# Kernel optimization log

Measured on AMD Instinct MI355X. Metric: run time of the kernel, lower is better.

The kernel has to match this reference:

```python
import jax, jax.numpy as jnp
import numpy as np

N = 50000
E = 800000
IN_C, HID, OUT_C, HEADS = 128, 32, 64, 4
NEG_SLOPE = 0.2


def setup_inputs() -> dict:
    key = jax.random.key(0)
    ks = jax.random.split(key, 10)
    x = jax.random.normal(ks[0], (N, IN_C), dtype=jnp.float32)
    edge_index = jax.random.randint(ks[1], (2, E), 0, N, dtype=jnp.int64)
    s = 0.05
    W1 = jax.random.normal(ks[2], (IN_C, HID), dtype=jnp.float32) * s
    b1 = jnp.zeros((HID,), dtype=jnp.float32)
    Wg = jax.random.normal(ks[3], (HID, HEADS * HID), dtype=jnp.float32) * s
    ag_src = jax.random.normal(ks[4], (HEADS, HID), dtype=jnp.float32) * s
    ag_dst = jax.random.normal(ks[5], (HEADS, HID), dtype=jnp.float32) * s
    bg = jnp.zeros((HID,), dtype=jnp.float32)
    W2 = jax.random.normal(ks[6], (HID, OUT_C), dtype=jnp.float32) * s
    b2 = jnp.zeros((OUT_C,), dtype=jnp.float32)
    return {"x": x, "edge_index": edge_index, "W1": W1, "b1": b1,
            "Wg": Wg, "ag_src": ag_src, "ag_dst": ag_dst, "bg": bg,
            "W2": W2, "b2": b2}


def _add_self_loops(edge_index, n):
    loop = jnp.arange(n, dtype=edge_index.dtype)
    return jnp.concatenate([edge_index, jnp.stack([loop, loop])], axis=1)


def _gcn(x, src, dst, W, b, n):
    # PyG GCNConv: symmetric normalization with self-loops, scatter-add
    xw = x @ W  # [N, F]
    deg = jnp.zeros((n,), xw.dtype).at[dst].add(1.0)  # in-degree incl self-loops
    dinv = jax.lax.rsqrt(deg)
    norm = dinv[src] * dinv[dst]  # [E']
    msg = xw[src] * norm[:, None]  # [E', F]
    out = jax.ops.segment_sum(msg, dst, num_segments=n)
    return out + b


def _gat(x, src, dst, Wg, a_src, a_dst, b, n):
    # PyG GATConv, concat=False (mean over heads), leaky_relu slope 0.2
    h = (x @ Wg).reshape(n, HEADS, HID)  # [N, H, D]
    al_s = jnp.einsum('nhd,hd->nh', h, a_src)  # [N, H]
    al_d = jnp.einsum('nhd,hd->nh', h, a_dst)
    logits = jax.nn.leaky_relu(al_s[src] + al_d[dst], NEG_SLOPE)  # [E', H]
    # segment softmax over incoming edges of each dst node
    m = jax.ops.segment_max(logits, dst, num_segments=n)
    e = jnp.exp(logits - m[dst])
    denom = jax.ops.segment_sum(e, dst, num_segments=n)
    alpha = e / denom[dst]  # [E', H]
    msg = h[src] * alpha[:, :, None]  # [E', H, D]
    out = jax.ops.segment_sum(msg, dst, num_segments=n)  # [N, H, D]
    return out.mean(axis=1) + b


def reference(x, edge_index, W1, b1, Wg, ag_src, ag_dst, bg, W2, b2):
    ei = _add_self_loops(edge_index, N)
    src, dst = ei[0], ei[1]
    h = jax.nn.relu(_gcn(x, src, dst, W1, b1, N))
    h = jax.nn.relu(_gat(h, src, dst, Wg, ag_src, ag_dst, bg, N))
    return _gcn(h, src, dst, W2, b2, N)
```

## Files before the change

kernel.cpp:

```cpp
#include <hip/hip_runtime.h>
#include <hip/hip_bf16.h>

#define N_NODES 50000
#define N_EDGES 800000
#define IN_C 128
#define HID 32
#define OUT_C 64
#define HEADS 4
#define NEG_SLOPE 0.2f

#define MAXDEG 64
#define N_PART 8
#define PART_W ((N_NODES + N_PART - 1) / N_PART)
#define FB 2048
#define RANKS (FB / N_PART)
#define EPB ((N_EDGES + RANKS - 1) / RANKS)
#define G1_TILES (N_NODES / 8)

typedef unsigned int uint32;
typedef unsigned short u16;
typedef __attribute__((ext_vector_type(8))) short bf16x8;
typedef __attribute__((ext_vector_type(4))) float f32x4;

__device__ __forceinline__ float bf_lo(uint32 u) { return __uint_as_float(u << 16); }
__device__ __forceinline__ float bf_hi(uint32 u) { return __uint_as_float(u & 0xffff0000u); }
__device__ __forceinline__ uint32 f2bf(float f) {
    uint32 u = __float_as_uint(f);
    return (u + 0x7fffu + ((u >> 16) & 1u)) >> 16;
}
__device__ __forceinline__ uint32 pack_bf2(float a, float b) {
    return f2bf(a) | (f2bf(b) << 16);
}

__global__ __launch_bounds__(256) void k_fused1(const float* __restrict__ x,
                                                const int* __restrict__ ei,
                                                int* __restrict__ ncnt,
                                                u16* __restrict__ srcs_pad,
                                                const float* __restrict__ W1,
                                                uint32* __restrict__ xw1,
                                                const float* __restrict__ Wg,
                                                const float* __restrict__ ags,
                                                const float* __restrict__ agd,
                                                float* __restrict__ wals,
                                                float* __restrict__ wald,
                                                const float* __restrict__ W2,
                                                uint32* __restrict__ wgB,
                                                uint32* __restrict__ w2B) {
    __shared__ float wl[IN_C * HID];
    __shared__ float xl[8 * IN_C];
    int t = threadIdx.x;
    for (int i = t; i < IN_C * HID; i += 256) {
        int k = i >> 5, f = i & 31;
        wl[(k >> 1) * 64 + f * 2 + (k & 1)] = W1[i];
    }
    __syncthreads();
    for (int tile = blockIdx.x; tile < G1_TILES; tile += FB) {
        int nb = tile * 8;
        const float4* x4 = (const float4*)(x + (size_t)nb * IN_C);
        ((float4*)xl)[t] = x4[t];
        __syncthreads();
        int g = t >> 5, f = t & 31;
        const float2* xr = (const float2*)(xl + g * IN_C);
        const float2* wp = (const float2*)wl;
        float acc = 0.f;
#pragma unroll 16
        for (int k2 = 0; k2 < 64; k2++) {
            float2 xv = xr[k2];
            float2 wv = wp[k2 * 32 + f];
            acc += xv.x * wv.x + xv.y * wv.y;
        }
        float vn = __shfl_xor(acc, 1, 64);
        if ((f & 1) == 0) xw1[(size_t)(nb + g) * 16 + (f >> 1)] = pack_bf2(acc, vn);
        __syncthreads();
    }
    if (blockIdx.x == 0) {
        {
            int c = t & 127;
            int h = c >> 5, k = c & 31;
            const float* a = (t < 128) ? ags : agd;
            float acc2 = 0.f;
#pragma unroll
            for (int d = 0; d < 32; d++) acc2 += Wg[k * 128 + h * 32 + d] * a[h * 32 + d];
            if (t < 128) wals[c] = acc2; else wald[c] = acc2;
        }
        for (int i = t; i < 2048; i += 256) {
            int tile = i >> 8;
            int T = tile >> 2, kt = tile & 3;
            int r = i & 255;
            int L = r >> 2, di = r & 3;
            int k0 = kt * 32 + (L >> 4) * 8 + 2 * di;
            int k1 = k0 + 1;
            int n = T * 16 + (L & 15);
            float a = Wg[(k0 & 31) * 128 + (k0 >> 5) * 32 + n];
            float b = Wg[(k1 & 31) * 128 + (k1 >> 5) * 32 + n];
            wgB[i] = pack_bf2(a, b);
        }
        for (int i = t; i < 1024; i += 256) {
            int T = i >> 8;
            int r = i & 255;
            int L = r >> 2, di = r & 3;
            int k0 = (L >> 4) * 8 + 2 * di;
            int n = T * 16 + (L & 15);
            w2B[i] = pack_bf2(W2[k0 * 64 + n], W2[(k0 + 1) * 64 + n]);
        }
    }
    {
        int part = blockIdx.x & (N_PART - 1);
        int rank = blockIdx.x >> 3;
        int lo = part * PART_W;
        int e0 = rank * EPB;
        int e1 = e0 + EPB; if (e1 > N_EDGES) e1 = N_EDGES;
        for (int e = e0 + t; e < e1; e += 256) {
            int d = ei[N_EDGES + e];
            if ((uint32)(d - lo) < (uint32)PART_W) {
                int s = ei[e];
                int pos = atomicAdd(&ncnt[d], 1);
                if (pos < MAXDEG) srcs_pad[(d << 6) + pos] = (u16)s;
            }
        }
    }
}

__global__ __launch_bounds__(256) void k_gather1(const uint32* __restrict__ xw1,
                                                 const int* __restrict__ ncnt,
                                                 const u16* __restrict__ srcs_pad,
                                                 const float* __restrict__ b1,
                                                 const float* __restrict__ wals,
                                                 const float* __restrict__ wald,
                                                 char* __restrict__ recH,
                                                 float* __restrict__ als,
                                                 float* __restrict__ ald) {
    __shared__ u16 s_src[16 * 64];
    int t = threadIdx.x;
    {
        const uint32* gsrc = (const uint32*)(srcs_pad + ((size_t)blockIdx.x * 16 << 6));
        ((uint32*)s_src)[t] = gsrc[t];
        ((uint32*)s_src)[t + 256] = gsrc[t + 256];
    }
    __syncthreads();
    int l16 = t & 15;
    int es = l16 >> 2;
    int q  = l16 & 3;
    int n = blockIdx.x * 16 + (t >> 4);
    int sbase = (t >> 4) << 6;
    int deg = ncnt[n];
    float a0 = 0.f, a1 = 0.f, a2 = 0.f, a3 = 0.f;
    float a4 = 0.f, a5 = 0.f, a6 = 0.f, a7 = 0.f;
#pragma unroll 2
    for (int jb = 0; jb <= deg; jb += 4) {
        int je = jb + es;
        if (je <= deg) {
            int sidx = (je < deg) ? (int)s_src[sbase + je] : n;
            float ws = rsqrtf((float)(ncnt[sidx] + 1));
            uint4 u = *(const uint4*)((const char*)xw1 + ((uint32)sidx << 6) + q * 16);
            a0 = fmaf(ws, bf_lo(u.x), a0); a1 = fmaf(ws, bf_hi(u.x), a1);
            a2 = fmaf(ws, bf_lo(u.y), a2); a3 = fmaf(ws, bf_hi(u.y), a3);
            a4 = fmaf(ws, bf_lo(u.z), a4); a5 = fmaf(ws, bf_hi(u.z), a5);
            a6 = fmaf(ws, bf_lo(u.w), a6); a7 = fmaf(ws, bf_hi(u.w), a7);
        }
    }
#define RED_ES(v) v += __shfl_xor(v, 4, 64); v += __shfl_xor(v, 8, 64);
    RED_ES(a0) RED_ES(a1) RED_ES(a2) RED_ES(a3)
    RED_ES(a4) RED_ES(a5) RED_ES(a6) RED_ES(a7)
#undef RED_ES
    float dn = rsqrtf((float)(deg + 1));
    float4 bA = ((const float4*)b1)[2 * q];
    float4 bB = ((const float4*)b1)[2 * q + 1];
    float v0 = a0 * dn + bA.x, v1 = a1 * dn + bA.y;
    float v2 = a2 * dn + bA.z, v3 = a3 * dn + bA.w;
    float v4 = a4 * dn + bB.x, v5 = a5 * dn + bB.y;
    float v6 = a6 * dn + bB.z, v7 = a7 * dn + bB.w;
    v0 = v0 > 0.f ? v0 : 0.f; v1 = v1 > 0.f ? v1 : 0.f;
    v2 = v2 > 0.f ? v2 : 0.f; v3 = v3 > 0.f ? v3 : 0.f;
    v4 = v4 > 0.f ? v4 : 0.f; v5 = v5 > 0.f ? v5 : 0.f;
    v6 = v6 > 0.f ? v6 : 0.f; v7 = v7 > 0.f ? v7 : 0.f;
    if (es == 0) {
        uint4 w;
        w.x = pack_bf2(v0, v1); w.y = pack_bf2(v2, v3);
        w.z = pack_bf2(v4, v5); w.w = pack_bf2(v6, v7);
        *(uint4*)(recH + ((uint32)n << 6) + q * 16) = w;
    }
    float ps[4], pd[4];
#pragma unroll
    for (int h = 0; h < 4; h++) {
        const float4* wa = (const float4*)(wals + h * 32 + 8 * q);
        float4 wv0 = wa[0], wv1 = wa[1];
        ps[h] = v0 * wv0.x + v1 * wv0.y + v2 * wv0.z + v3 * wv0.w
              + v4 * wv1.x + v5 * wv1.y + v6 * wv1.z + v7 * wv1.w;
        const float4* wb = (const float4*)(wald + h * 32 + 8 * q);
        float4 uv0 = wb[0], uv1 = wb[1];
        pd[h] = v0 * uv0.x + v1 * uv0.y + v2 * uv0.z + v3 * uv0.w
              + v4 * uv1.x + v5 * uv1.y + v6 * uv1.z + v7 * uv1.w;
    }
#pragma unroll
    for (int h = 0; h < 4; h++) {
        ps[h] += __shfl_xor(ps[h], 1, 64); ps[h] += __shfl_xor(ps[h], 2, 64);
        pd[h] += __shfl_xor(pd[h], 1, 64); pd[h] += __shfl_xor(pd[h], 2, 64);
    }
    if (l16 == 0) {
        ((float4*)als)[n] = make_float4(ps[0], ps[1], ps[2], ps[3]);
        ((float4*)ald)[n] = make_float4(pd[0], pd[1], pd[2], pd[3]);
    }
}

__global__ __launch_bounds__(512) void k_gat_agg(const char* __restrict__ recH,
                                                 const float* __restrict__ als,
                                                 const float* __restrict__ ald,
                                                 const int* __restrict__ ncnt,
                                                 const u16* __restrict__ srcs_pad,
                                                 const uint32* __restrict__ wgB,
                                                 const float* __restrict__ bg,
                                                 uint32* __restrict__ h2s) {
    __shared__ __align__(16) uint32 gl[16][64];
    __shared__ u16 s_src[16 * 64];
    int t = threadIdx.x;
    {
        const uint32* gsrc = (const uint32*)(srcs_pad + ((size_t)blockIdx.x * 16 << 6));
        ((uint32*)s_src)[t] = gsrc[t];
    }
    __syncthreads();
    int l32 = t & 31;
    int g8 = t >> 5;
    int n = blockIdx.x * 16 + g8;
    int es = l32 >> 3;
    int q  = l32 & 7;
    int sbase = g8 << 6;
    int deg = ncnt[n];
    float4 dv = ((const float4*)ald)[n];

    float g00 = 0.f, g01 = 0.f, g02 = 0.f, g03 = 0.f;
    float g10 = 0.f, g11 = 0.f, g12 = 0.f, g13 = 0.f;
    float g20 = 0.f, g21 = 0.f, g22 = 0.f, g23 = 0.f;
    float g30 = 0.f, g31 = 0.f, g32 = 0.f, g33 = 0.f;
    float ss0 = 0.f, ss1 = 0.f, ss2 = 0.f, ss3 = 0.f;

#pragma unroll 2
    for (int jb = 0; jb <= deg; jb += 4) {
        int je = jb + es;
        if (je <= deg) {
            int sidx = (je < deg) ? (int)s_src[sbase + je] : n;
            float4 ev = ((const float4*)als)[sidx];
            uint2 u = *(const uint2*)(recH + ((uint32)sidx << 6) + q * 8);
            float f0 = bf_lo(u.x), f1 = bf_hi(u.x);
            float f2 = bf_lo(u.y), f3 = bf_hi(u.y);
            float tt, w;
            tt = ev.x + dv.x; w = __expf(fmaxf(tt, NEG_SLOPE * tt));
            ss0 += w; g00 += w * f0; g01 += w * f1; g02 += w * f2; g03 += w * f3;
            tt = ev.y + dv.y; w = __expf(fmaxf(tt, NEG_SLOPE * tt));
            ss1 += w; g10 += w * f0; g11 += w * f1; g12 += w * f2; g13 += w * f3;
            tt = ev.z + dv.z; w = __expf(fmaxf(tt, NEG_SLOPE * tt));
            ss2 += w; g20 += w * f0; g21 += w * f1; g22 += w * f2; g23 += w * f3;
            tt = ev.w + dv.w; w = __expf(fmaxf(tt, NEG_SLOPE * tt));
            ss3 += w; g30 += w * f0; g31 += w * f1; g32 += w * f2; g33 += w * f3;
        }
    }
#define RED_ES(v) v += __shfl_xor(v, 8, 64); v += __shfl_xor(v, 16, 64);
    RED_ES(ss0) RED_ES(ss1) RED_ES(ss2) RED_ES(ss3)
    RED_ES(g00) RED_ES(g01) RED_ES(g02) RED_ES(g03)
    RED_ES(g10) RED_ES(g11) RED_ES(g12) RED_ES(g13)
    RED_ES(g20) RED_ES(g21) RED_ES(g22) RED_ES(g23)
    RED_ES(g30) RED_ES(g31) RED_ES(g32) RED_ES(g33)
#undef RED_ES
    float i0 = 0.25f / ss0, i1 = 0.25f / ss1, i2 = 0.25f / ss2, i3 = 0.25f / ss3;
    if (es == 0) {
        uint2 w;
        w.x = pack_bf2(g00 * i0, g01 * i0); w.y = pack_bf2(g02 * i0, g03 * i0);
        *(uint2*)&gl[g8][0 * 16 + 2 * q] = w;
        w.x = pack_bf2(g10 * i1, g11 * i1); w.y = pack_bf2(g12 * i1, g13 * i1);
        *(uint2*)&gl[g8][1 * 16 + 2 * q] = w;
        w.x = pack_bf2(g20 * i2, g21 * i2); w.y = pack_bf2(g22 * i2, g23 * i2);
        *(uint2*)&gl[g8][2 * 16 + 2 * q] = w;
        w.x = pack_bf2(g30 * i3, g31 * i3); w.y = pack_bf2(g32 * i3, g33 * i3);
        *(uint2*)&gl[g8][3 * 16 + 2 * q] = w;
    }
    __syncthreads();
    if (t < 64) {
        int L = t;
        int mA = L & 15;
        int quad = L >> 4;
        int nbase = blockIdx.x * 16;
        float dns[4];
#pragma unroll
        for (int r = 0; r < 4; r++)
            dns[r] = rsqrtf((float)(ncnt[nbase + quad * 4 + r] + 1));
#pragma unroll
        for (int T = 0; T < 2; T++) {
            f32x4 acc = {0.f, 0.f, 0.f, 0.f};
#pragma unroll
            for (int kt = 0; kt < 4; kt++) {
                bf16x8 af = *(const bf16x8*)&gl[mA][kt * 16 + quad * 4];
                bf16x8 bf = *(const bf16x8*)(wgB + (size_t)((T * 4 + kt) * 64 + L) * 4);
                acc = __builtin_amdgcn_mfma_f32_16x16x32_bf16(af, bf, acc, 0, 0, 0);
            }
            int d = T * 16 + (L & 15);
            float bgd = bg[d];
#pragma unroll
            for (int r = 0; r < 4; r++) {
                int node = nbase + quad * 4 + r;
                float v = acc[r] + bgd;
                v = v > 0.f ? v : 0.f;
                v *= dns[r];
                float vn = __shfl_xor(v, 1, 64);
                if ((d & 1) == 0)
                    h2s[(size_t)node * 16 + (d >> 1)] = pack_bf2(v, vn);
            }
        }
    }
}

__global__ __launch_bounds__(256) void k_gather2(const uint32* __restrict__ h2s,
                                                 const int* __restrict__ ncnt,
                                                 const u16* __restrict__ srcs_pad,
                                                 const uint32* __restrict__ w2B,
                                                 const float* __restrict__ b2,
                                                 float* __restrict__ out) {
    __shared__ __align__(16) uint32 gbf[16][16];
    __shared__ u16 s_src[16 * 64];
    int t = threadIdx.x;
    {
        const uint32* gsrc = (const uint32*)(srcs_pad + ((size_t)blockIdx.x * 16 << 6));
        ((uint32*)s_src)[t] = gsrc[t];
        ((uint32*)s_src)[t + 256] = gsrc[t + 256];
    }
    __syncthreads();
    int l16 = t & 15;
    int es = l16 >> 2;
    int q  = l16 & 3;
    int g16 = t >> 4;
    int n = blockIdx.x * 16 + g16;
    int sbase = g16 << 6;
    int deg = ncnt[n];
    float a0 = 0.f, a1 = 0.f, a2 = 0.f, a3 = 0.f;
    float a4 = 0.f, a5 = 0.f, a6 = 0.f, a7 = 0.f;
#pragma unroll 2
    for (int jb = 0; jb <= deg; jb += 4) {
        int je = jb + es;
        if (je <= deg) {
            int sidx = (je < deg) ? (int)s_src[sbase + je] : n;
            uint4 u = *(const uint4*)((const char*)h2s + ((uint32)sidx << 6) + q * 16);
            a0 += bf_lo(u.x); a1 += bf_hi(u.x);
            a2 += bf_lo(u.y); a3 += bf_hi(u.y);
            a4 += bf_lo(u.z); a5 += bf_hi(u.z);
            a6 += bf_lo(u.w); a7 += bf_hi(u.w);
        }
    }
#define RED_ES(v) v += __shfl_xor(v, 4, 64); v += __shfl_xor(v, 8, 64);
    RED_ES(a0) RED_ES(a1) RED_ES(a2) RED_ES(a3)
    RED_ES(a4) RED_ES(a5) RED_ES(a6) RED_ES(a7)
#undef RED_ES
    if (es == 0) {
        uint4 w;
        w.x = pack_bf2(a0, a1); w.y = pack_bf2(a2, a3);
        w.z = pack_bf2(a4, a5); w.w = pack_bf2(a6, a7);
        *(uint4*)&gbf[g16][4 * q] = w;
    }
    __syncthreads();
    if (t < 64) {
        int L = t;
        int quad = L >> 4;
        int nbase = blockIdx.x * 16;
        float dns[4];
#pragma unroll
        for (int r = 0; r < 4; r++)
            dns[r] = rsqrtf((float)(ncnt[nbase + quad * 4 + r] + 1));
        bf16x8 af = *(const bf16x8*)&gbf[L & 15][quad * 4];
#pragma unroll
        for (int T = 0; T < 4; T++) {
            bf16x8 bf = *(const bf16x8*)(w2B + (size_t)(T * 64 + L) * 4);
            f32x4 acc = {0.f, 0.f, 0.f, 0.f};
            acc = __builtin_amdgcn_mfma_f32_16x16x32_bf16(af, bf, acc, 0, 0, 0);
            int d = T * 16 + (L & 15);
            float b2d = b2[d];
#pragma unroll
            for (int r = 0; r < 4; r++) {
                int node = nbase + quad * 4 + r;
                out[(size_t)node * OUT_C + d] = acc[r] * dns[r] + b2d;
            }
        }
    }
}

extern "C" void kernel_launch(void* const* d_in, const int* in_sizes, int n_in,
                              void* d_out, int out_size, void* d_ws, size_t ws_size,
                              hipStream_t stream) {
    const float* x   = (const float*)d_in[0];
    const int*   ei  = (const int*)d_in[1];
    const float* W1  = (const float*)d_in[2];
    const float* b1  = (const float*)d_in[3];
    const float* Wg  = (const float*)d_in[4];
    const float* ags = (const float*)d_in[5];
    const float* agd = (const float*)d_in[6];
    const float* bg  = (const float*)d_in[7];
    const float* W2  = (const float*)d_in[8];
    const float* b2  = (const float*)d_in[9];
    float* out = (float*)d_out;

    char* p = (char*)d_ws;
    auto alloc = [&](size_t bytes) -> void* {
        void* r = (void*)p;
        p += (bytes + 255) & ~(size_t)255;
        return r;
    };
    int*    ncnt     = (int*)   alloc((size_t)N_NODES * 4);
    u16*    srcs_pad = (u16*)   alloc((size_t)N_NODES * MAXDEG * 2);
    uint32* xw1      = (uint32*)alloc((size_t)N_NODES * 16 * 4);
    char*   recH     = (char*)  alloc((size_t)N_NODES * 64);
    float*  als      = (float*) alloc((size_t)N_NODES * 4 * 4);
    float*  ald      = (float*) alloc((size_t)N_NODES * 4 * 4);
    float*  wals     = (float*) alloc(128 * 4);
    float*  wald     = (float*) alloc(128 * 4);
    uint32* wgB      = (uint32*)alloc(2048 * 4);
    uint32* w2B      = (uint32*)alloc(1024 * 4);
    uint32* h2s      = (uint32*)alloc((size_t)N_NODES * 16 * 4);

    hipMemsetAsync(ncnt, 0, (size_t)N_NODES * 4, stream);

    k_fused1<<<FB, 256, 0, stream>>>(x, ei, ncnt, srcs_pad, W1, xw1,
                                     Wg, ags, agd, wals, wald, W2, wgB, w2B);

    k_gather1<<<N_NODES / 16, 256, 0, stream>>>(xw1, ncnt, srcs_pad, b1,
                                                wals, wald, recH, als, ald);

    k_gat_agg<<<N_NODES / 16, 512, 0, stream>>>(recH, als, ald, ncnt, srcs_pad,
                                                wgB, bg, h2s);

    k_gather2<<<N_NODES / 16, 256, 0, stream>>>(h2s, ncnt, srcs_pad, w2B, b2, out);
}
```

Before: 196.2 us.

## Prescale GCN source rows and widen gathers to eight edge slots per node

Adds a small kernel that multiplies each xw1 row by its source node's rsqrt degree ahead of time. This removes the per-edge ncnt lookup and rsqrt from the first gather. Both gather kernels now use 32 threads per node (8 edge slots instead of 4) with 512-thread blocks, plus an extra shuffle step in the reduction. In exchange there is an extra launch, a read-modify-write pass over xw1, and a second bf16 rounding of the scaled values.

```diff
diff --git a/kernel.cpp b/kernel.cpp
--- a/kernel.cpp
+++ b/kernel.cpp
@@ -121,7 +121,15 @@
     }
 }
 
-__global__ __launch_bounds__(256) void k_gather1(const uint32* __restrict__ xw1,
+__global__ __launch_bounds__(256) void k_scale(uint32* __restrict__ xw1,
+                                               const int* __restrict__ ncnt) {
+    int i = blockIdx.x * 256 + threadIdx.x;
+    uint32 u = xw1[i];
+    float dn = rsqrtf((float)(ncnt[i >> 4] + 1));
+    xw1[i] = pack_bf2(bf_lo(u) * dn, bf_hi(u) * dn);
+}
+
+__global__ __launch_bounds__(512) void k_gather1(const uint32* __restrict__ xw1,
                                                  const int* __restrict__ ncnt,
                                                  const u16* __restrict__ srcs_pad,
                                                  const float* __restrict__ b1,
@@ -135,31 +143,30 @@
     {
         const uint32* gsrc = (const uint32*)(srcs_pad + ((size_t)blockIdx.x * 16 << 6));
         ((uint32*)s_src)[t] = gsrc[t];
-        ((uint32*)s_src)[t + 256] = gsrc[t + 256];
-    }
-    __syncthreads();
-    int l16 = t & 15;
-    int es = l16 >> 2;
-    int q  = l16 & 3;
-    int n = blockIdx.x * 16 + (t >> 4);
-    int sbase = (t >> 4) << 6;
+    }
+    __syncthreads();
+    int l32 = t & 31;
+    int es = l32 >> 2;
+    int q  = l32 & 3;
+    int n = blockIdx.x * 16 + (t >> 5);
+    int sbase = (t >> 5) << 6;
     int deg = ncnt[n];
     float a0 = 0.f, a1 = 0.f, a2 = 0.f, a3 = 0.f;
     float a4 = 0.f, a5 = 0.f, a6 = 0.f, a7 = 0.f;
 #pragma unroll 2
-    for (int jb = 0; jb <= deg; jb += 4) {
+    for (int jb = 0; jb <= deg; jb += 8) {
         int je = jb + es;
         if (je <= deg) {
             int sidx = (je < deg) ? (int)s_src[sbase + je] : n;
-            float ws = rsqrtf((float)(ncnt[sidx] + 1));
             uint4 u = *(const uint4*)((const char*)xw1 + ((uint32)sidx << 6) + q * 16);
-            a0 = fmaf(ws, bf_lo(u.x), a0); a1 = fmaf(ws, bf_hi(u.x), a1);
-            a2 = fmaf(ws, bf_lo(u.y), a2); a3 = fmaf(ws, bf_hi(u.y), a3);
-            a4 = fmaf(ws, bf_lo(u.z), a4); a5 = fmaf(ws, bf_hi(u.z), a5);
-            a6 = fmaf(ws, bf_lo(u.w), a6); a7 = fmaf(ws, bf_hi(u.w), a7);
-        }
-    }
-#define RED_ES(v) v += __shfl_xor(v, 4, 64); v += __shfl_xor(v, 8, 64);
+            a0 += bf_lo(u.x); a1 += bf_hi(u.x);
+            a2 += bf_lo(u.y); a3 += bf_hi(u.y);
+            a4 += bf_lo(u.z); a5 += bf_hi(u.z);
+            a6 += bf_lo(u.w); a7 += bf_hi(u.w);
+        }
+    }
+#define RED_ES(v) v += __shfl_xor(v, 4, 64); v += __shfl_xor(v, 8, 64); \
+                  v += __shfl_xor(v, 16, 64);
     RED_ES(a0) RED_ES(a1) RED_ES(a2) RED_ES(a3)
     RED_ES(a4) RED_ES(a5) RED_ES(a6) RED_ES(a7)
 #undef RED_ES
@@ -197,7 +204,7 @@
         ps[h] += __shfl_xor(ps[h], 1, 64); ps[h] += __shfl_xor(ps[h], 2, 64);
         pd[h] += __shfl_xor(pd[h], 1, 64); pd[h] += __shfl_xor(pd[h], 2, 64);
     }
-    if (l16 == 0) {
+    if (l32 == 0) {
         ((float4*)als)[n] = make_float4(ps[0], ps[1], ps[2], ps[3]);
         ((float4*)ald)[n] = make_float4(pd[0], pd[1], pd[2], pd[3]);
     }
@@ -308,7 +315,7 @@
     }
 }
 
-__global__ __launch_bounds__(256) void k_gather2(const uint32* __restrict__ h2s,
+__global__ __launch_bounds__(512) void k_gather2(const uint32* __restrict__ h2s,
                                                  const int* __restrict__ ncnt,
                                                  const u16* __restrict__ srcs_pad,
                                                  const uint32* __restrict__ w2B,
@@ -320,20 +327,19 @@
     {
         const uint32* gsrc = (const uint32*)(srcs_pad + ((size_t)blockIdx.x * 16 << 6));
         ((uint32*)s_src)[t] = gsrc[t];
-        ((uint32*)s_src)[t + 256] = gsrc[t + 256];
-    }
-    __syncthreads();
-    int l16 = t & 15;
-    int es = l16 >> 2;
-    int q  = l16 & 3;
-    int g16 = t >> 4;
+    }
+    __syncthreads();
+    int l32 = t & 31;
+    int es = l32 >> 2;
+    int q  = l32 & 3;
+    int g16 = t >> 5;
     int n = blockIdx.x * 16 + g16;
     int sbase = g16 << 6;
     int deg = ncnt[n];
     float a0 = 0.f, a1 = 0.f, a2 = 0.f, a3 = 0.f;
     float a4 = 0.f, a5 = 0.f, a6 = 0.f, a7 = 0.f;
 #pragma unroll 2
-    for (int jb = 0; jb <= deg; jb += 4) {
+    for (int jb = 0; jb <= deg; jb += 8) {
         int je = jb + es;
         if (je <= deg) {
             int sidx = (je < deg) ? (int)s_src[sbase + je] : n;
@@ -344,7 +350,8 @@
             a6 += bf_lo(u.w); a7 += bf_hi(u.w);
         }
     }
-#define RED_ES(v) v += __shfl_xor(v, 4, 64); v += __shfl_xor(v, 8, 64);
+#define RED_ES(v) v += __shfl_xor(v, 4, 64); v += __shfl_xor(v, 8, 64); \
+                  v += __shfl_xor(v, 16, 64);
     RED_ES(a0) RED_ES(a1) RED_ES(a2) RED_ES(a3)
     RED_ES(a4) RED_ES(a5) RED_ES(a6) RED_ES(a7)
 #undef RED_ES
@@ -418,11 +425,13 @@
     k_fused1<<<FB, 256, 0, stream>>>(x, ei, ncnt, srcs_pad, W1, xw1,
                                      Wg, ags, agd, wals, wald, W2, wgB, w2B);
 
-    k_gather1<<<N_NODES / 16, 256, 0, stream>>>(xw1, ncnt, srcs_pad, b1,
+    k_scale<<<(N_NODES * 16) / 256, 256, 0, stream>>>(xw1, ncnt);
+
+    k_gather1<<<N_NODES / 16, 512, 0, stream>>>(xw1, ncnt, srcs_pad, b1,
                                                 wals, wald, recH, als, ald);
 
     k_gat_agg<<<N_NODES / 16, 512, 0, stream>>>(recH, als, ald, ncnt, srcs_pad,
                                                 wgB, bg, h2s);
 
-    k_gather2<<<N_NODES / 16, 256, 0, stream>>>(h2s, ncnt, srcs_pad, w2B, b2, out);
-}
+    k_gather2<<<N_NODES / 16, 512, 0, stream>>>(h2s, ncnt, srcs_pad, w2B, b2, out);
+}
```

New measurement: 206.3 us. 5.2% more time.
